# Kernel optimization log

Hardware: AMD Instinct MI355X
Metric: run time of the kernel (lower is better)

The kernel has to match this reference:

```python
import jax, jax.numpy as jnp
import numpy as np

N = 50000
E = 800000
N_IN = 256
N_HID = 128
N_OUT = 64
HOP = 10


def setup_inputs() -> dict:
    key = jax.random.key(0)
    ks = jax.random.split(key, 12)
    x = jax.random.normal(ks[0], (N, N_IN), dtype=jnp.float32)
    s = jax.random.randint(ks[1], (E,), 0, N, dtype=jnp.int32)
    t = jax.random.randint(ks[2], (E,), 0, N, dtype=jnp.int32)
    # parameters (xavier-ish scaling)
    fc1W = jax.random.normal(ks[3], (N_HID, N_IN), dtype=jnp.float32) * (1.0 / np.sqrt(N_IN))
    fc1b = jnp.zeros((N_HID,), dtype=jnp.float32)
    fcsW = jax.random.normal(ks[4], (HOP, N_HID, N_HID), dtype=jnp.float32) * (1.0 / np.sqrt(N_HID))
    fcsb = jnp.zeros((HOP, N_HID), dtype=jnp.float32)
    a1 = jax.random.normal(ks[5], (HOP, N_HID), dtype=jnp.float32) * (1.0 / np.sqrt(N_HID))
    a2 = jax.random.normal(ks[6], (HOP, N_HID), dtype=jnp.float32) * (1.0 / np.sqrt(N_HID))
    fc2W = jax.random.normal(ks[7], (N_OUT, N_HID), dtype=jnp.float32) * (1.0 / np.sqrt(N_HID))
    fc2b = jnp.zeros((N_OUT,), dtype=jnp.float32)
    return {"x": x, "s": s, "t": t, "fc1W": fc1W, "fc1b": fc1b,
            "fcsW": fcsW, "fcsb": fcsb, "a1": a1, "a2": a2,
            "fc2W": fc2W, "fc2b": fc2b}


def reference(x, s, t, fc1W, fc1b, fcsW, fcsb, a1, a2, fc2W, fc2b):
    # dropout layers are identity in eval mode
    x = jax.nn.relu(x @ fc1W.T + fc1b)  # [N, n_hid]
    h = x
    for i in range(HOP):
        W, b = fcsW[i], fcsb[i]
        x_new = x @ W.T + b          # [N, n_hid]
        h = h @ W.T + b              # [N, n_hid]
        x1 = x_new @ a1[i]           # [N]
        h1 = h @ a2[i]               # [N]
        w1 = jnp.exp(jax.nn.leaky_relu(x1[s] + h1[t], 0.2))       # [E]
        w2 = jnp.exp(jax.nn.leaky_relu(x1 + x_new @ a2[i], 0.2))  # [N]
        div = jax.ops.segment_sum(w1, s, num_segments=N) + w2     # [N]
        num = jax.ops.segment_sum(w1[:, None] * h[t], s, num_segments=N) + w2[:, None] * x_new
        h = jax.nn.elu(num / div[:, None])
    return h @ fc2W.T + fc2b  # [N, n_out]
```

## Files before the change

kernel.cpp:

```cpp
#include <hip/hip_runtime.h>
#include <math.h>


typedef __attribute__((ext_vector_type(8))) short short8;
typedef __attribute__((ext_vector_type(4))) float f32x4;
#define MFMA16 __builtin_amdgcn_mfma_f32_16x16x32_bf16

__device__ __forceinline__ float lrelu02(float v) { return v > 0.f ? v : 0.2f * v; }

__device__ __forceinline__ float2 bf2f2(unsigned int v) {
    return make_float2(__uint_as_float(v << 16), __uint_as_float(v & 0xffff0000u));
}
__device__ __forceinline__ unsigned int f2bf(float f) {
    unsigned int u = __float_as_uint(f);
    u += 0x7fffu + ((u >> 16) & 1u);
    return u >> 16;
}
__device__ __forceinline__ float hi_part(float f) {
    return __uint_as_float(__float_as_uint(f) & 0xffff0000u);
}
__device__ __forceinline__ uint4 pack_hi(const float4& a, const float4& b) {
    uint4 r;
    r.x = (__float_as_uint(a.x) >> 16) | (__float_as_uint(a.y) & 0xffff0000u);
    r.y = (__float_as_uint(a.z) >> 16) | (__float_as_uint(a.w) & 0xffff0000u);
    r.z = (__float_as_uint(b.x) >> 16) | (__float_as_uint(b.y) & 0xffff0000u);
    r.w = (__float_as_uint(b.z) >> 16) | (__float_as_uint(b.w) & 0xffff0000u);
    return r;
}
__device__ __forceinline__ uint4 pack_lo(const float4& a, const float4& b) {
    uint4 r;
    r.x = f2bf(a.x - hi_part(a.x)) | (f2bf(a.y - hi_part(a.y)) << 16);
    r.y = f2bf(a.z - hi_part(a.z)) | (f2bf(a.w - hi_part(a.w)) << 16);
    r.z = f2bf(b.x - hi_part(b.x)) | (f2bf(b.y - hi_part(b.y)) << 16);
    r.w = f2bf(b.z - hi_part(b.z)) | (f2bf(b.w - hi_part(b.w)) << 16);
    return r;
}

__global__ __launch_bounds__(256) void k_count(const int* __restrict__ s, int* __restrict__ cnt, int E) {
    int e = blockIdx.x * 256 + threadIdx.x;
    if (e < E) atomicAdd(&cnt[s[e]], 1);
}

__global__ __launch_bounds__(256) void k_scan1(const int* __restrict__ cnt, int* __restrict__ bs, int N) {
    __shared__ int sh[256];
    int idx = blockIdx.x * 256 + threadIdx.x;
    sh[threadIdx.x] = (idx < N) ? cnt[idx] : 0;
    __syncthreads();
#pragma unroll
    for (int off = 128; off; off >>= 1) {
        if (threadIdx.x < off) sh[threadIdx.x] += sh[threadIdx.x + off];
        __syncthreads();
    }
    if (threadIdx.x == 0) bs[blockIdx.x] = sh[0];
}

__global__ __launch_bounds__(256) void k_scan2(int* __restrict__ bs, int G) {
    __shared__ int sh[256];
    int t = threadIdx.x;
    int v = (t < G) ? bs[t] : 0;
    sh[t] = v;
    __syncthreads();
    int val = v;
#pragma unroll
    for (int off = 1; off < 256; off <<= 1) {
        int o = (t >= off) ? sh[t - off] : 0;
        __syncthreads();
        val += o; sh[t] = val;
        __syncthreads();
    }
    if (t < G) bs[t] = val - v;
}

__global__ __launch_bounds__(256) void k_scan3(const int* __restrict__ cnt, const int* __restrict__ bs,
                                               int* __restrict__ rp, int N) {
    __shared__ int sh[256];
    int t = threadIdx.x;
    int idx = blockIdx.x * 256 + t;
    int v = (idx < N) ? cnt[idx] : 0;
    sh[t] = v;
    __syncthreads();
    int val = v;
#pragma unroll
    for (int off = 1; off < 256; off <<= 1) {
        int o = (t >= off) ? sh[t - off] : 0;
        __syncthreads();
        val += o; sh[t] = val;
        __syncthreads();
    }
    if (idx <= N) rp[idx] = val - v + bs[blockIdx.x];
}

__global__ __launch_bounds__(256) void k_scatter(const int* __restrict__ s, const int* __restrict__ t,
                                                 const int* __restrict__ rp, int* __restrict__ cursor,
                                                 int* __restrict__ t_sorted, int E) {
    int e = blockIdx.x * 256 + threadIdx.x;
    if (e < E) {
        int u = s[e];
        int pos = atomicAdd(&cursor[u], 1);
        t_sorted[rp[u] + pos] = t[e];
    }
}

__global__ __launch_bounds__(256) void k_wsplit(const float* __restrict__ W,
                                                unsigned short* __restrict__ Whi,
                                                unsigned short* __restrict__ Wlo, int total) {
    int i = blockIdx.x * 256 + threadIdx.x;
    if (i < total) {
        float f = W[i];
        unsigned int u = __float_as_uint(f);
        Whi[i] = (unsigned short)(u >> 16);
        Wlo[i] = (unsigned short)f2bf(f - __uint_as_float(u & 0xffff0000u));
    }
}

template <int MODE>
__global__ __launch_bounds__(256) void k_mmfc(
    const float* __restrict__ Xf,
    const unsigned short* __restrict__ Xhi,
    const float* __restrict__ Wf, const float* __restrict__ bias,
    float* __restrict__ Yf, unsigned short* __restrict__ Yhi, unsigned short* __restrict__ Ylo,
    int N) {
    constexpr int K = (MODE == 1) ? 256 : 128;
    constexpr int NCOLS = (MODE == 1) ? 128 : 64;
    __shared__ unsigned short lds[2 * 128 * 64];
    unsigned short* Xs = lds;
    unsigned short* Wt = lds + 128 * 64;

    const int tid = threadIdx.x;
    const int r0 = blockIdx.x * 128;
    const int srow = tid & 127;
    const int sp = tid >> 7;
    const int xrow = r0 + srow;
    const bool xok = xrow < N;
    const bool wok = srow < NCOLS;

    const int lane = tid & 63;
    const int w = tid >> 6;
    const int wr = (w >> 1) * 64, wc = (w & 1) * 64;
    const int frow = lane & 15;
    const int fk = lane >> 4;
    const int q4 = lane >> 4;

    f32x4 acc[4][4];
#pragma unroll
    for (int i = 0; i < 4; ++i)
#pragma unroll
        for (int j = 0; j < 4; ++j) acc[i][j] = (f32x4){0.f, 0.f, 0.f, 0.f};

    const float4 z4 = make_float4(0.f, 0.f, 0.f, 0.f);
    const uint4 zz = make_uint4(0, 0, 0, 0);

    for (int kc = 0; kc < K / 32; ++kc) {
        if constexpr (MODE == 1) {
            const float* xp = Xf + (size_t)xrow * K + kc * 32 + sp * 16;
            const float* wp = Wf + (size_t)srow * K + kc * 32 + sp * 16;
            float4 xv[4], wv[4];
#pragma unroll
            for (int q = 0; q < 4; ++q) {
                xv[q] = xok ? *(const float4*)(xp + q * 4) : z4;
                wv[q] = wok ? *(const float4*)(wp + q * 4) : z4;
            }
            __syncthreads();
#pragma unroll
            for (int j = 0; j < 2; ++j) {
                int g = sp * 2 + j;
                *(uint4*)(Xs + srow * 64 + ((g) ^ (srow & 7)) * 8)     = pack_hi(xv[2 * j], xv[2 * j + 1]);
                *(uint4*)(Xs + srow * 64 + ((4 | g) ^ (srow & 7)) * 8) = pack_lo(xv[2 * j], xv[2 * j + 1]);
                *(uint4*)(Wt + srow * 64 + ((g) ^ (srow & 7)) * 8)     = pack_hi(wv[2 * j], wv[2 * j + 1]);
                *(uint4*)(Wt + srow * 64 + ((4 | g) ^ (srow & 7)) * 8) = pack_lo(wv[2 * j], wv[2 * j + 1]);
            }
            __syncthreads();
        } else {
            const unsigned short* xp = Xhi + (size_t)xrow * K + kc * 32;
            const float* wp = Wf + (size_t)srow * K + kc * 32 + sp * 16;
            uint4 xg[4];
            float4 wv[4];
#pragma unroll
            for (int g = 0; g < 4; ++g) xg[g] = (xok && sp == 0) ? ((const uint4*)xp)[g] : zz;
#pragma unroll
            for (int q = 0; q < 4; ++q) wv[q] = wok ? *(const float4*)(wp + q * 4) : z4;
            __syncthreads();
            if (sp == 0) {
#pragma unroll
                for (int g = 0; g < 4; ++g) {
                    int p = g ^ (srow & 7);
                    *(uint4*)(Xs + srow * 64 + p * 8) = xg[g];
                }
            }
#pragma unroll
            for (int j = 0; j < 2; ++j) {
                int g = sp * 2 + j;
                *(uint4*)(Wt + srow * 64 + ((g) ^ (srow & 7)) * 8)     = pack_hi(wv[2 * j], wv[2 * j + 1]);
                *(uint4*)(Wt + srow * 64 + ((4 | g) ^ (srow & 7)) * 8) = pack_lo(wv[2 * j], wv[2 * j + 1]);
            }
            __syncthreads();
        }

        short8 ah[4], bh[4], bl[4];
#pragma unroll
        for (int ri = 0; ri < 4; ++ri) {
            int row = wr + ri * 16 + frow;
            ah[ri] = *(const short8*)(Xs + row * 64 + ((fk) ^ (row & 7)) * 8);
        }
#pragma unroll
        for (int ci = 0; ci < 4; ++ci) {
            int col = wc + ci * 16 + frow;
            bh[ci] = *(const short8*)(Wt + col * 64 + ((fk) ^ (col & 7)) * 8);
            bl[ci] = *(const short8*)(Wt + col * 64 + ((4 | fk) ^ (col & 7)) * 8);
        }
        if constexpr (MODE == 1) {
            short8 al[4];
#pragma unroll
            for (int ri = 0; ri < 4; ++ri) {
                int row = wr + ri * 16 + frow;
                al[ri] = *(const short8*)(Xs + row * 64 + ((4 | fk) ^ (row & 7)) * 8);
            }
#pragma unroll
            for (int ri = 0; ri < 4; ++ri)
#pragma unroll
                for (int ci = 0; ci < 4; ++ci) {
                    acc[ri][ci] = MFMA16(ah[ri], bh[ci], acc[ri][ci], 0, 0, 0);
                    acc[ri][ci] = MFMA16(ah[ri], bl[ci], acc[ri][ci], 0, 0, 0);
                    acc[ri][ci] = MFMA16(al[ri], bh[ci], acc[ri][ci], 0, 0, 0);
                }
        } else {
#pragma unroll
            for (int ri = 0; ri < 4; ++ri)
#pragma unroll
                for (int ci = 0; ci < 4; ++ci) {
                    acc[ri][ci] = MFMA16(ah[ri], bh[ci], acc[ri][ci], 0, 0, 0);
                    acc[ri][ci] = MFMA16(ah[ri], bl[ci], acc[ri][ci], 0, 0, 0);
                }
        }
    }

#pragma unroll
    for (int ci = 0; ci < 4; ++ci) {
        int col = wc + ci * 16 + frow;
        float bcol = (col < NCOLS) ? bias[col] : 0.f;
#pragma unroll
        for (int ri = 0; ri < 4; ++ri) {
            f32x4 v = acc[ri][ci];
#pragma unroll
            for (int reg = 0; reg < 4; ++reg) {
                int grow = r0 + wr + ri * 16 + q4 * 4 + reg;
                float val = v[reg] + bcol;
                if (grow < N && col < NCOLS) {
                    if constexpr (MODE == 1) {
                        val = fmaxf(val, 0.f);
                        Yhi[(size_t)grow * 128 + col] = (unsigned short)(__float_as_uint(val) >> 16);
                        Ylo[(size_t)grow * 128 + col] = (unsigned short)f2bf(val - hi_part(val));
                    } else {
                        Yf[(size_t)grow * 64 + col] = val;
                    }
                }
            }
        }
    }
}

__global__ __launch_bounds__(256) void k_mm_bf(
    const unsigned short* __restrict__ Xhi0, const unsigned short* __restrict__ Xlo0, int nblk0,
    const unsigned short* __restrict__ Hhi1,
    const unsigned short* __restrict__ Whi, const unsigned short* __restrict__ Wlo,
    const float* __restrict__ bias,
    unsigned short* __restrict__ Yb0, unsigned short* __restrict__ Yb1, int N,
    const float* __restrict__ dA0, float* __restrict__ oA0,
    const float* __restrict__ dB0, float* __restrict__ oB0,
    const float* __restrict__ dA1, float* __restrict__ oA1) {
    __shared__ unsigned short lds[2 * 128 * 128];

    const int tid = threadIdx.x;
    const bool second = (int)blockIdx.x >= nblk0;
    const int bx = second ? (int)blockIdx.x - nblk0 : (int)blockIdx.x;
    const int r0 = bx * 128;

    {
        int col = tid & 127;
        int pl = tid >> 7;
        const unsigned short* wp = (pl ? Wlo : Whi) + (size_t)col * 128;
        unsigned short* dst = lds + pl * 16384 + col * 128;
#pragma unroll
        for (int g = 0; g < 16; ++g)
            *(uint4*)(dst + ((g ^ (col & 7)) * 8)) = ((const uint4*)wp)[g];
    }
    __syncthreads();

    const int lane = tid & 63;
    const int w = tid >> 6;
    const int wr = (w >> 1) * 64, wc = (w & 1) * 64;
    const int frow = lane & 15;
    const int fk = lane >> 4;
    const int q4 = lane >> 4;

    const unsigned short* Xh = second ? Hhi1 : Xhi0;
    const unsigned short* Xl = Xlo0;
    unsigned short* Yb = second ? Yb1 : Yb0;

    f32x4 acc[4][4];
#pragma unroll
    for (int i = 0; i < 4; ++i)
#pragma unroll
        for (int j = 0; j < 4; ++j) acc[i][j] = (f32x4){0.f, 0.f, 0.f, 0.f};

    const short8 z8 = (short8){0, 0, 0, 0, 0, 0, 0, 0};

#pragma unroll
    for (int kc = 0; kc < 4; ++kc) {
        short8 ah[4], al[4], bh[4], bl[4];
#pragma unroll
        for (int ri = 0; ri < 4; ++ri) {
            int row = r0 + wr + ri * 16 + frow;
            bool ok = row < N;
            const unsigned short* ph = Xh + (size_t)row * 128 + kc * 32 + fk * 8;
            ah[ri] = ok ? *(const short8*)ph : z8;
            if (!second) {
                const unsigned short* pl = Xl + (size_t)row * 128 + kc * 32 + fk * 8;
                al[ri] = ok ? *(const short8*)pl : z8;
            }
        }
#pragma unroll
        for (int ci = 0; ci < 4; ++ci) {
            int col = wc + ci * 16 + frow;
            int g = kc * 4 + fk;
            int go = (g ^ (col & 7)) * 8;
            bh[ci] = *(const short8*)(lds + col * 128 + go);
            bl[ci] = *(const short8*)(lds + 16384 + col * 128 + go);
        }
        if (!second) {
#pragma unroll
            for (int ri = 0; ri < 4; ++ri)
#pragma unroll
                for (int ci = 0; ci < 4; ++ci) {
                    acc[ri][ci] = MFMA16(ah[ri], bh[ci], acc[ri][ci], 0, 0, 0);
                    acc[ri][ci] = MFMA16(ah[ri], bl[ci], acc[ri][ci], 0, 0, 0);
                    acc[ri][ci] = MFMA16(al[ri], bh[ci], acc[ri][ci], 0, 0, 0);
                }
        } else {
#pragma unroll
            for (int ri = 0; ri < 4; ++ri)
#pragma unroll
                for (int ci = 0; ci < 4; ++ci) {
                    acc[ri][ci] = MFMA16(ah[ri], bh[ci], acc[ri][ci], 0, 0, 0);
                    acc[ri][ci] = MFMA16(ah[ri], bl[ci], acc[ri][ci], 0, 0, 0);
                }
        }
    }

    const float* dA = second ? dA1 : dA0;
    const float* dB = second ? nullptr : dB0;
    unsigned short* So = lds;
    float* dotbuf = (float*)(lds + 16384);

    float dotA[4][4] = {}, dotB[4][4] = {};
    __syncthreads();
#pragma unroll
    for (int ci = 0; ci < 4; ++ci) {
        int col = wc + ci * 16 + frow;
        float bcol = bias[col];
        float dAc = dA ? dA[col] : 0.f;
        float dBc = dB ? dB[col] : 0.f;
#pragma unroll
        for (int ri = 0; ri < 4; ++ri) {
            f32x4 v = acc[ri][ci];
#pragma unroll
            for (int reg = 0; reg < 4; ++reg) {
                float val = v[reg] + bcol;
                int row = wr + ri * 16 + q4 * 4 + reg;
                int dw = (col >> 1) ^ ((row & 12) << 1);
                So[row * 128 + dw * 2 + (col & 1)] = (unsigned short)f2bf(val);
                dotA[ri][reg] = fmaf(val, dAc, dotA[ri][reg]);
                dotB[ri][reg] = fmaf(val, dBc, dotB[ri][reg]);
            }
        }
    }
#pragma unroll
    for (int m = 1; m < 16; m <<= 1)
#pragma unroll
        for (int ri = 0; ri < 4; ++ri)
#pragma unroll
            for (int reg = 0; reg < 4; ++reg) {
                dotA[ri][reg] += __shfl_xor(dotA[ri][reg], m, 64);
                dotB[ri][reg] += __shfl_xor(dotB[ri][reg], m, 64);
            }
    if (frow == 0) {
#pragma unroll
        for (int ri = 0; ri < 4; ++ri)
#pragma unroll
            for (int reg = 0; reg < 4; ++reg) {
                int rl = wr + ri * 16 + q4 * 4 + reg;
                dotbuf[(0 * 128 + rl) * 2 + (w & 1)] = dotA[ri][reg];
                dotbuf[(1 * 128 + rl) * 2 + (w & 1)] = dotB[ri][reg];
            }
    }
    __syncthreads();

#pragma unroll
    for (int q = 0; q < 8; ++q) {
        int idx = q * 256 + tid;
        int row = idx >> 4;
        int gc = idx & 15;
        int dwb = (gc * 4) ^ ((row & 12) << 1);
        uint4 vv = *(const uint4*)(So + row * 128 + dwb * 2);
        int grow = r0 + row;
        if (grow < N) *(uint4*)(Yb + (size_t)grow * 128 + gc * 8) = vv;
    }
    {
        int d = tid >> 7, rl = tid & 127;
        int grow = r0 + rl;
        float* oA = second ? oA1 : oA0;
        float* oB = second ? nullptr : oB0;
        if (grow < N) {
            float v = dotbuf[(d * 128 + rl) * 2] + dotbuf[(d * 128 + rl) * 2 + 1];
            if (d == 0) { if (oA) oA[grow] = v; }
            else        { if (oB) oB[grow] = v; }
        }
    }
}

__global__ __launch_bounds__(256) void k_agg(
    const unsigned short* __restrict__ xnb, const unsigned short* __restrict__ hbf,
    const float* __restrict__ x1a, const float* __restrict__ xa2a,
    const float* __restrict__ h1a, const int* __restrict__ rp,
    const int* __restrict__ ts,
    unsigned short* __restrict__ hhi, int N) {
    __shared__ uint2 ew[4][64];
    const int wid = threadIdx.x >> 6;
    const int lane = threadIdx.x & 63;
    const int u = blockIdx.x * 4 + wid;
    if (u >= N) return;
    const int l2 = lane << 1;
    float x1u = x1a[u];
    float w2 = expf(lrelu02(x1u + xa2a[u]));
    float2 xr = bf2f2(*(const unsigned int*)(xnb + (size_t)u * 128 + l2));
    float accx = w2 * xr.x, accy = w2 * xr.y;
    float div = w2;
    int p0 = rp[u], p1 = rp[u + 1];
    for (int base = p0; base < p1; base += 64) {
        int e = base + lane;
        uint2 pk = make_uint2(0u, 0u);
        if (e < p1) {
            int tv = ts[e];
            pk.x = (unsigned int)tv;
            pk.y = __float_as_uint(expf(lrelu02(x1u + h1a[tv])));
        }
        ew[wid][lane] = pk;
        int m = p1 - base; if (m > 64) m = 64;
        int m8 = (m + 7) & ~7;
        for (int j = 0; j < m8; j += 8) {
            uint2 q[8];
#pragma unroll
            for (int k = 0; k < 8; ++k) q[k] = ew[wid][j + k];
            unsigned int hv[8];
#pragma unroll
            for (int k = 0; k < 8; ++k)
                hv[k] = *(const unsigned int*)(hbf + (size_t)q[k].x * 128 + l2);
#pragma unroll
            for (int k = 0; k < 8; ++k) {
                float ww = __uint_as_float(q[k].y);
                float2 f = bf2f2(hv[k]);
                accx = fmaf(ww, f.x, accx);
                accy = fmaf(ww, f.y, accy);
                div += ww;
            }
        }
    }
    float ox = accx / div, oy = accy / div;
    ox = ox > 0.f ? ox : expf(ox) - 1.f;
    oy = oy > 0.f ? oy : expf(oy) - 1.f;
    unsigned int hx = __float_as_uint(ox), hy = __float_as_uint(oy);
    *(unsigned int*)(hhi + (size_t)u * 128 + l2) = (hx >> 16) | (hy & 0xffff0000u);
}

extern "C" void kernel_launch(void* const* d_in, const int* in_sizes, int n_in,
                              void* d_out, int out_size, void* d_ws, size_t ws_size,
                              hipStream_t stream) {
    const float* x_in = (const float*)d_in[0];
    const int*   s    = (const int*)d_in[1];
    const int*   t    = (const int*)d_in[2];
    const float* fc1W = (const float*)d_in[3];
    const float* fc1b = (const float*)d_in[4];
    const float* fcsW = (const float*)d_in[5];
    const float* fcsb = (const float*)d_in[6];
    const float* a1   = (const float*)d_in[7];
    const float* a2   = (const float*)d_in[8];
    const float* fc2W = (const float*)d_in[9];
    const float* fc2b = (const float*)d_in[10];

    const int N = in_sizes[0] / 256;
    const int E = in_sizes[1];
    const int G = (N + 255) / 256;
    const int NB = (N + 127) / 128;

    char* ws = (char*)d_ws;
    size_t off = 0;
    auto alloc = [&](size_t bytes) -> void* {
        void* p = ws + off;
        off += (bytes + 255) & ~(size_t)255;
        return p;
    };
    unsigned short* xbuf_hi = (unsigned short*)alloc((size_t)N * 128 * 2);
    unsigned short* xbuf_lo = (unsigned short*)alloc((size_t)N * 128 * 2);
    unsigned short* h_hi    = (unsigned short*)alloc((size_t)N * 128 * 2);
    unsigned short* xnb     = (unsigned short*)alloc((size_t)N * 128 * 2);
    unsigned short* hbf     = (unsigned short*)alloc((size_t)N * 128 * 2);
    unsigned short* Whi = (unsigned short*)alloc((size_t)10 * 128 * 128 * 2);
    unsigned short* Wlo = (unsigned short*)alloc((size_t)10 * 128 * 128 * 2);
    float* x1a  = (float*)alloc((size_t)N * 4);
    float* xa2a = (float*)alloc((size_t)N * 4);
    float* h1a  = (float*)alloc((size_t)N * 4);
    int* row_ptr  = (int*)alloc((size_t)(N + 1) * 4);
    int* cnt      = (int*)alloc((size_t)N * 4);
    int* bsums    = (int*)alloc((size_t)256 * 4);
    int* t_sorted = (int*)alloc((size_t)E * 4);

    hipMemsetAsync(cnt, 0, (size_t)N * 4, stream);
    k_count<<<(E + 255) / 256, 256, 0, stream>>>(s, cnt, E);
    k_scan1<<<G, 256, 0, stream>>>(cnt, bsums, N);
    k_scan2<<<1, 256, 0, stream>>>(bsums, G);
    k_scan3<<<G, 256, 0, stream>>>(cnt, bsums, row_ptr, N);
    hipMemsetAsync(cnt, 0, (size_t)N * 4, stream);
    k_scatter<<<(E + 255) / 256, 256, 0, stream>>>(s, t, row_ptr, cnt, t_sorted, E);

    k_wsplit<<<(10 * 128 * 128 + 255) / 256, 256, 0, stream>>>(fcsW, Whi, Wlo, 10 * 128 * 128);

    k_mmfc<1><<<NB, 256, 0, stream>>>(x_in, nullptr, fc1W, fc1b,
                                      nullptr, xbuf_hi, xbuf_lo, N);

    for (int i = 0; i < 10; ++i) {
        const unsigned short* Wh = Whi + (size_t)i * 128 * 128;
        const unsigned short* Wl = Wlo + (size_t)i * 128 * 128;
        const float* b   = fcsb + (size_t)i * 128;
        const float* a1i = a1 + (size_t)i * 128;
        const float* a2i = a2 + (size_t)i * 128;
        if (i == 0) {
            k_mm_bf<<<NB, 256, 0, stream>>>(xbuf_hi, xbuf_lo, NB, h_hi,
                                            Wh, Wl, b, xnb, hbf, N,
                                            a1i, x1a, a2i, xa2a, a2i, h1a);
            k_agg<<<(N + 3) / 4, 256, 0, stream>>>(xnb, xnb, x1a, xa2a, xa2a,
                                                   row_ptr, t_sorted, h_hi, N);
        } else {
            k_mm_bf<<<2 * NB, 256, 0, stream>>>(xbuf_hi, xbuf_lo, NB, h_hi,
                                                Wh, Wl, b, xnb, hbf, N,
                                                a1i, x1a, a2i, xa2a, a2i, h1a);
            k_agg<<<(N + 3) / 4, 256, 0, stream>>>(xnb, hbf, x1a, xa2a, h1a,
                                                   row_ptr, t_sorted, h_hi, N);
        }
    }

    k_mmfc<2><<<NB, 256, 0, stream>>>(nullptr, h_hi, fc2W, fc2b,
                                      (float*)d_out, nullptr, nullptr, N);
}
```

Baseline: 879.4 us.

## Replace LDS-staged fc1/fc2 GEMMs with direct-register MFMA loads and pre-split weights

The templated fc1/fc2 kernel is split into two kernels that load MFMA fragments straight from global memory into registers, with no LDS staging and no __syncthreads. fc1W and fc2W are split into bf16 hi/lo halves once by extra k_wsplit launches instead of being packed per tile. fc2 gets its own 64-row tiling so that no wave idles on the 64 output columns. The aim is to remove LDS round-trips and barriers, at the cost of redundant global/L2 loads of the input rows and weights across waves.

After: 859.5 us. -2.3%, faster.

```diff
diff --git a/kernel.cpp b/kernel.cpp
--- a/kernel.cpp
+++ b/kernel.cpp
@@ -113,27 +113,13 @@
     }
 }
 
-template <int MODE>
-__global__ __launch_bounds__(256) void k_mmfc(
+__global__ __launch_bounds__(256) void k_fc1(
     const float* __restrict__ Xf,
-    const unsigned short* __restrict__ Xhi,
-    const float* __restrict__ Wf, const float* __restrict__ bias,
-    float* __restrict__ Yf, unsigned short* __restrict__ Yhi, unsigned short* __restrict__ Ylo,
-    int N) {
-    constexpr int K = (MODE == 1) ? 256 : 128;
-    constexpr int NCOLS = (MODE == 1) ? 128 : 64;
-    __shared__ unsigned short lds[2 * 128 * 64];
-    unsigned short* Xs = lds;
-    unsigned short* Wt = lds + 128 * 64;
-
+    const unsigned short* __restrict__ Wh, const unsigned short* __restrict__ Wl,
+    const float* __restrict__ bias,
+    unsigned short* __restrict__ Yhi, unsigned short* __restrict__ Ylo, int N) {
     const int tid = threadIdx.x;
     const int r0 = blockIdx.x * 128;
-    const int srow = tid & 127;
-    const int sp = tid >> 7;
-    const int xrow = r0 + srow;
-    const bool xok = xrow < N;
-    const bool wok = srow < NCOLS;
-
     const int lane = tid & 63;
     const int w = tid >> 6;
     const int wr = (w >> 1) * 64, wc = (w & 1) * 64;
@@ -148,113 +134,97 @@
         for (int j = 0; j < 4; ++j) acc[i][j] = (f32x4){0.f, 0.f, 0.f, 0.f};
 
     const float4 z4 = make_float4(0.f, 0.f, 0.f, 0.f);
-    const uint4 zz = make_uint4(0, 0, 0, 0);
-
-    for (int kc = 0; kc < K / 32; ++kc) {
-        if constexpr (MODE == 1) {
-            const float* xp = Xf + (size_t)xrow * K + kc * 32 + sp * 16;
-            const float* wp = Wf + (size_t)srow * K + kc * 32 + sp * 16;
-            float4 xv[4], wv[4];
-#pragma unroll
-            for (int q = 0; q < 4; ++q) {
-                xv[q] = xok ? *(const float4*)(xp + q * 4) : z4;
-                wv[q] = wok ? *(const float4*)(wp + q * 4) : z4;
-            }
-            __syncthreads();
-#pragma unroll
-            for (int j = 0; j < 2; ++j) {
-                int g = sp * 2 + j;
-                *(uint4*)(Xs + srow * 64 + ((g) ^ (srow & 7)) * 8)     = pack_hi(xv[2 * j], xv[2 * j + 1]);
-                *(uint4*)(Xs + srow * 64 + ((4 | g) ^ (srow & 7)) * 8) = pack_lo(xv[2 * j], xv[2 * j + 1]);
-                *(uint4*)(Wt + srow * 64 + ((g) ^ (srow & 7)) * 8)     = pack_hi(wv[2 * j], wv[2 * j + 1]);
-                *(uint4*)(Wt + srow * 64 + ((4 | g) ^ (srow & 7)) * 8) = pack_lo(wv[2 * j], wv[2 * j + 1]);
-            }
-            __syncthreads();
-        } else {
-            const unsigned short* xp = Xhi + (size_t)xrow * K + kc * 32;
-            const float* wp = Wf + (size_t)srow * K + kc * 32 + sp * 16;
-            uint4 xg[4];
-            float4 wv[4];
-#pragma unroll
-            for (int g = 0; g < 4; ++g) xg[g] = (xok && sp == 0) ? ((const uint4*)xp)[g] : zz;
-#pragma unroll
-            for (int q = 0; q < 4; ++q) wv[q] = wok ? *(const float4*)(wp + q * 4) : z4;
-            __syncthreads();
-            if (sp == 0) {
-#pragma unroll
-                for (int g = 0; g < 4; ++g) {
-                    int p = g ^ (srow & 7);
-                    *(uint4*)(Xs + srow * 64 + p * 8) = xg[g];
-                }
-            }
-#pragma unroll
-            for (int j = 0; j < 2; ++j) {
-                int g = sp * 2 + j;
-                *(uint4*)(Wt + srow * 64 + ((g) ^ (srow & 7)) * 8)     = pack_hi(wv[2 * j], wv[2 * j + 1]);
-                *(uint4*)(Wt + srow * 64 + ((4 | g) ^ (srow & 7)) * 8) = pack_lo(wv[2 * j], wv[2 * j + 1]);
-            }
-            __syncthreads();
-        }
-
-        short8 ah[4], bh[4], bl[4];
+#pragma unroll
+    for (int kc = 0; kc < 8; ++kc) {
+        short8 ah[4], al[4];
 #pragma unroll
         for (int ri = 0; ri < 4; ++ri) {
-            int row = wr + ri * 16 + frow;
-            ah[ri] = *(const short8*)(Xs + row * 64 + ((fk) ^ (row & 7)) * 8);
+            int row = r0 + wr + ri * 16 + frow;
+            float4 va = z4, vb = z4;
+            if (row < N) {
+                const float* p = Xf + (size_t)row * 256 + kc * 32 + fk * 8;
+                va = *(const float4*)p;
+                vb = *(const float4*)(p + 4);
+            }
+            uint4 h = pack_hi(va, vb);
+            uint4 l = pack_lo(va, vb);
+            ah[ri] = *(short8*)&h;
+            al[ri] = *(short8*)&l;
         }
 #pragma unroll
         for (int ci = 0; ci < 4; ++ci) {
             int col = wc + ci * 16 + frow;
-            bh[ci] = *(const short8*)(Wt + col * 64 + ((fk) ^ (col & 7)) * 8);
-            bl[ci] = *(const short8*)(Wt + col * 64 + ((4 | fk) ^ (col & 7)) * 8);
-        }
-        if constexpr (MODE == 1) {
-            short8 al[4];
+            short8 bh = *(const short8*)(Wh + (size_t)col * 256 + kc * 32 + fk * 8);
+            short8 bl = *(const short8*)(Wl + (size_t)col * 256 + kc * 32 + fk * 8);
 #pragma unroll
             for (int ri = 0; ri < 4; ++ri) {
-                int row = wr + ri * 16 + frow;
-                al[ri] = *(const short8*)(Xs + row * 64 + ((4 | fk) ^ (row & 7)) * 8);
-            }
-#pragma unroll
-            for (int ri = 0; ri < 4; ++ri)
-#pragma unroll
-                for (int ci = 0; ci < 4; ++ci) {
-                    acc[ri][ci] = MFMA16(ah[ri], bh[ci], acc[ri][ci], 0, 0, 0);
-                    acc[ri][ci] = MFMA16(ah[ri], bl[ci], acc[ri][ci], 0, 0, 0);
-                    acc[ri][ci] = MFMA16(al[ri], bh[ci], acc[ri][ci], 0, 0, 0);
-                }
-        } else {
-#pragma unroll
-            for (int ri = 0; ri < 4; ++ri)
-#pragma unroll
-                for (int ci = 0; ci < 4; ++ci) {
-                    acc[ri][ci] = MFMA16(ah[ri], bh[ci], acc[ri][ci], 0, 0, 0);
-                    acc[ri][ci] = MFMA16(ah[ri], bl[ci], acc[ri][ci], 0, 0, 0);
-                }
+                acc[ri][ci] = MFMA16(ah[ri], bh, acc[ri][ci], 0, 0, 0);
+                acc[ri][ci] = MFMA16(ah[ri], bl, acc[ri][ci], 0, 0, 0);
+                acc[ri][ci] = MFMA16(al[ri], bh, acc[ri][ci], 0, 0, 0);
+            }
         }
     }
 
 #pragma unroll
     for (int ci = 0; ci < 4; ++ci) {
         int col = wc + ci * 16 + frow;
-        float bcol = (col < NCOLS) ? bias[col] : 0.f;
+        float bcol = bias[col];
 #pragma unroll
         for (int ri = 0; ri < 4; ++ri) {
             f32x4 v = acc[ri][ci];
 #pragma unroll
             for (int reg = 0; reg < 4; ++reg) {
                 int grow = r0 + wr + ri * 16 + q4 * 4 + reg;
-                float val = v[reg] + bcol;
-                if (grow < N && col < NCOLS) {
-                    if constexpr (MODE == 1) {
-                        val = fmaxf(val, 0.f);
-                        Yhi[(size_t)grow * 128 + col] = (unsigned short)(__float_as_uint(val) >> 16);
-                        Ylo[(size_t)grow * 128 + col] = (unsigned short)f2bf(val - hi_part(val));
-                    } else {
-                        Yf[(size_t)grow * 64 + col] = val;
-                    }
+                if (grow < N) {
+                    float val = fmaxf(v[reg] + bcol, 0.f);
+                    Yhi[(size_t)grow * 128 + col] = (unsigned short)(__float_as_uint(val) >> 16);
+                    Ylo[(size_t)grow * 128 + col] = (unsigned short)f2bf(val - hi_part(val));
                 }
             }
+        }
+    }
+}
+
+__global__ __launch_bounds__(256) void k_fc2(
+    const unsigned short* __restrict__ Xhi,
+    const unsigned short* __restrict__ Wh, const unsigned short* __restrict__ Wl,
+    const float* __restrict__ bias, float* __restrict__ Yf, int N) {
+    const int tid = threadIdx.x;
+    const int r0 = blockIdx.x * 64;
+    const int lane = tid & 63;
+    const int w = tid >> 6;
+    const int wr = w * 16;
+    const int frow = lane & 15;
+    const int fk = lane >> 4;
+    const int q4 = lane >> 4;
+
+    f32x4 acc[4];
+#pragma unroll
+    for (int j = 0; j < 4; ++j) acc[j] = (f32x4){0.f, 0.f, 0.f, 0.f};
+
+    const short8 z8 = (short8){0, 0, 0, 0, 0, 0, 0, 0};
+#pragma unroll
+    for (int kc = 0; kc < 4; ++kc) {
+        int row = r0 + wr + frow;
+        short8 ah = (row < N) ? *(const short8*)(Xhi + (size_t)row * 128 + kc * 32 + fk * 8) : z8;
+#pragma unroll
+        for (int ci = 0; ci < 4; ++ci) {
+            int col = ci * 16 + frow;
+            short8 bh = *(const short8*)(Wh + (size_t)col * 128 + kc * 32 + fk * 8);
+            short8 bl = *(const short8*)(Wl + (size_t)col * 128 + kc * 32 + fk * 8);
+            acc[ci] = MFMA16(ah, bh, acc[ci], 0, 0, 0);
+            acc[ci] = MFMA16(ah, bl, acc[ci], 0, 0, 0);
+        }
+    }
+
+#pragma unroll
+    for (int ci = 0; ci < 4; ++ci) {
+        int col = ci * 16 + frow;
+        float bcol = bias[col];
+#pragma unroll
+        for (int reg = 0; reg < 4; ++reg) {
+            int grow = r0 + wr + q4 * 4 + reg;
+            if (grow < N) Yf[(size_t)grow * 64 + col] = acc[ci][reg] + bcol;
         }
     }
 }
@@ -504,8 +474,12 @@
     unsigned short* h_hi    = (unsigned short*)alloc((size_t)N * 128 * 2);
     unsigned short* xnb     = (unsigned short*)alloc((size_t)N * 128 * 2);
     unsigned short* hbf     = (unsigned short*)alloc((size_t)N * 128 * 2);
-    unsigned short* Whi = (unsigned short*)alloc((size_t)10 * 128 * 128 * 2);
-    unsigned short* Wlo = (unsigned short*)alloc((size_t)10 * 128 * 128 * 2);
+    unsigned short* Whi  = (unsigned short*)alloc((size_t)10 * 128 * 128 * 2);
+    unsigned short* Wlo  = (unsigned short*)alloc((size_t)10 * 128 * 128 * 2);
+    unsigned short* W1hi = (unsigned short*)alloc((size_t)128 * 256 * 2);
+    unsigned short* W1lo = (unsigned short*)alloc((size_t)128 * 256 * 2);
+    unsigned short* W2hi = (unsigned short*)alloc((size_t)64 * 128 * 2);
+    unsigned short* W2lo = (unsigned short*)alloc((size_t)64 * 128 * 2);
     float* x1a  = (float*)alloc((size_t)N * 4);
     float* xa2a = (float*)alloc((size_t)N * 4);
     float* h1a  = (float*)alloc((size_t)N * 4);
@@ -523,9 +497,10 @@
     k_scatter<<<(E + 255) / 256, 256, 0, stream>>>(s, t, row_ptr, cnt, t_sorted, E);
 
     k_wsplit<<<(10 * 128 * 128 + 255) / 256, 256, 0, stream>>>(fcsW, Whi, Wlo, 10 * 128 * 128);
-
-    k_mmfc<1><<<NB, 256, 0, stream>>>(x_in, nullptr, fc1W, fc1b,
-                                      nullptr, xbuf_hi, xbuf_lo, N);
+    k_wsplit<<<(128 * 256 + 255) / 256, 256, 0, stream>>>(fc1W, W1hi, W1lo, 128 * 256);
+    k_wsplit<<<(64 * 128 + 255) / 256, 256, 0, stream>>>(fc2W, W2hi, W2lo, 64 * 128);
+
+    k_fc1<<<NB, 256, 0, stream>>>(x_in, W1hi, W1lo, fc1b, xbuf_hi, xbuf_lo, N);
 
     for (int i = 0; i < 10; ++i) {
         const unsigned short* Wh = Whi + (size_t)i * 128 * 128;
@@ -548,6 +523,5 @@
         }
     }
 
-    k_mmfc<2><<<NB, 256, 0, stream>>>(nullptr, h_hi, fc2W, fc2b,
-                                      (float*)d_out, nullptr, nullptr, N);
-}
+    k_fc2<<<(N + 63) / 64, 256, 0, stream>>>(h_hi, W2hi, W2lo, fc2b, (float*)d_out, N);
+}
```
